# Performance work log

Measured on AMD Instinct MI355X. Metric: run time of the kernel, lower is better.

## Reference

```python
import jax, jax.numpy as jnp
import numpy as np


def setup_inputs() -> dict:
    key = jax.random.key(0)
    ks = jax.random.split(key, 5)
    B, T, I, H = 64, 512, 1024, 1024
    s = 1.0 / np.sqrt(H)
    return {
        "x": jax.random.normal(ks[0], (B, T, I), dtype=jnp.float32),
        "w_ih": jax.random.normal(ks[1], (4 * H, I), dtype=jnp.float32) * s,
        "b_ih": jax.random.normal(ks[2], (4 * H,), dtype=jnp.float32) * s,
        "w_hh": jax.random.normal(ks[3], (4 * H, H), dtype=jnp.float32) * s,
        "b_hh": jax.random.normal(ks[4], (4 * H,), dtype=jnp.float32) * s,
    }


def _lstm(x, w_ih, b_ih, w_hh, b_hh):
    B, T, _ = x.shape
    H = w_hh.shape[1]
    # Precompute input projections for all timesteps: [T, B, 4H]
    gx = jnp.einsum("bti,gi->tbg", x, w_ih) + b_ih
    h0 = jnp.zeros((B, H), dtype=x.dtype)
    c0 = jnp.zeros((B, H), dtype=x.dtype)

    def step(carry, g_x):
        h, c = carry
        gates = g_x + h @ w_hh.T + b_hh  # [B, 4H]
        i_lin, f_lin, g_lin, o_lin = jnp.split(gates, 4, axis=-1)
        i = jax.nn.sigmoid(i_lin)
        f = jax.nn.sigmoid(f_lin)
        g = jnp.tanh(g_lin)
        o = jax.nn.sigmoid(o_lin)
        c = f * c + i * g
        h = o * jnp.tanh(c)
        return (h, c), h

    (hT, cT), hs = jax.lax.scan(step, (h0, c0), gx)
    output = jnp.transpose(hs, (1, 0, 2))  # [B, T, H]
    hn = hT[None, :, :]  # [1, B, H]
    cn = cT[None, :, :]
    return output, hn, cn


def reference(x, w_ih, b_ih, w_hh, b_hh):
    return _lstm(x, w_ih, b_ih, w_hh, b_hh)
```

## Files before the change

### kernel.cpp

```cpp
#include <hip/hip_runtime.h>
#include <hip/hip_bf16.h>

#define Bv 64
#define Tv 512
#define Iv 1024
#define Hv 1024
#define G4v 4096
#define BH (Bv * Hv)
#define NHB 64
#define NXB 128
#define NBLK (NHB + NXB)
#define DEPTH 8
#define FSTR 16

typedef __attribute__((ext_vector_type(8))) short bf16x8;
typedef __attribute__((ext_vector_type(4))) float f32x4;

#define LOADC(p)    __hip_atomic_load((p), __ATOMIC_RELAXED, __HIP_MEMORY_SCOPE_AGENT)
#define STOREC(p,v) __hip_atomic_store((p), (v), __ATOMIC_RELAXED, __HIP_MEMORY_SCOPE_AGENT)

__device__ __forceinline__ float sigmoid_f(float v) { return 1.f / (1.f + __expf(-v)); }
__device__ __forceinline__ float tanh_f(float v) { return 1.f - 2.f / (__expf(2.f * v) + 1.f); }

__device__ __forceinline__ void store_short_sc1(void* p, unsigned short v) {
  asm volatile("global_store_short %0, %1, off sc1" :: "v"(p), "v"((unsigned)v) : "memory");
}

__global__ void prep(const float* __restrict__ w_ih, const float* __restrict__ w_hh,
                     const float* __restrict__ b_ih, const float* __restrict__ b_hh,
                     __hip_bfloat16* __restrict__ wbih, __hip_bfloat16* __restrict__ wbhh,
                     float* __restrict__ bias, __hip_bfloat16* __restrict__ hbuf,
                     unsigned* __restrict__ hflag, unsigned* __restrict__ xflag) {
  unsigned i = blockIdx.x * 256u + threadIdx.x;
  wbih[i] = __float2bfloat16(w_ih[i]);
  wbhh[i] = __float2bfloat16(w_hh[i]);
  if (i < (unsigned)G4v) bias[i] = b_ih[i] + b_hh[i];
  if (i < 2u * BH) hbuf[i] = __float2bfloat16(0.f);
  if (i < (unsigned)(NHB * FSTR)) hflag[i] = 0u;
  if (i < (unsigned)(NXB * FSTR)) xflag[i] = 0u;
}

__global__ void __launch_bounds__(256, 1) lstm_main(
    const float* __restrict__ x,
    const __hip_bfloat16* __restrict__ wbih,
    const __hip_bfloat16* __restrict__ wbhh,
    const float* __restrict__ bias,
    __hip_bfloat16* __restrict__ hbuf,
    float* __restrict__ xg,
    float* __restrict__ out,
    unsigned* __restrict__ hflag,
    unsigned* __restrict__ xflag,
    int ring)
{
  extern __shared__ char lds[];

  const int bid  = blockIdx.x;
  const bool is_h = (bid < NHB);
  const int tid  = threadIdx.x;
  const int lane = tid & 63;
  const int wave = tid >> 6;
  const int lrow = lane & 15;
  const int lkg  = lane >> 4;
  const int lk   = lkg * 8;

  const int wg = is_h ? bid : ((bid - NHB) >> 1);
  const int rh = is_h ? 0 : ((bid - NHB) & 1);

  {
    const __hip_bfloat16* wsrc = is_h ? wbhh : wbih;
    for (int c = tid; c < 8192; c += 256) {
      int n   = c >> 7;
      int k16 = c & 127;
      int gc  = ((n >> 4) << 10) + (wg << 4) + (n & 15);
      uint4 v = *(const uint4*)(wsrc + ((size_t)gc << 10) + (k16 << 3));
      unsigned byt = (unsigned)((n << 11) + (k16 << 4)) ^ ((unsigned)(n & 7) << 4);
      *(uint4*)(&lds[byt]) = v;
    }
  }
  __syncthreads();

  if (!is_h) {
    const int j  = bid - NHB;
    const int wr = wave & 1;
    const int wc = wave >> 1;
    const int arow = rh * 32 + wr * 16 + lrow;
    const float* xa = x + (size_t)arow * (Tv * Iv) + lk;

    for (int t = 0; t < Tv; ++t) {
      if (t >= DEPTH) {
        if (wave == 0) {
          const unsigned tgt = (unsigned)(t - DEPTH + 1);
          for (;;) {
            unsigned hf = LOADC(&hflag[lane * FSTR]);
            if (__all(hf >= tgt)) break;
            __builtin_amdgcn_s_sleep(4);
          }
        }
        __syncthreads();
        asm volatile("" ::: "memory");
      }
      f32x4 acc[2];
      acc[0] = f32x4{0.f,0.f,0.f,0.f}; acc[1] = f32x4{0.f,0.f,0.f,0.f};
      const float* xt = xa + (size_t)t * Iv;
      #pragma unroll 4
      for (int ks = 0; ks < 32; ++ks) {
        int k0 = (ks << 5) + lk;
        float4 f0 = *(const float4*)(xt + (ks << 5));
        float4 f1 = *(const float4*)(xt + (ks << 5) + 4);
        union { __hip_bfloat16 e[8]; bf16x8 v; } u;
        u.e[0] = __float2bfloat16(f0.x); u.e[1] = __float2bfloat16(f0.y);
        u.e[2] = __float2bfloat16(f0.z); u.e[3] = __float2bfloat16(f0.w);
        u.e[4] = __float2bfloat16(f1.x); u.e[5] = __float2bfloat16(f1.y);
        u.e[6] = __float2bfloat16(f1.z); u.e[7] = __float2bfloat16(f1.w);
        bf16x8 b0, b1;
        {
          int n = wc * 32 + lrow;
          unsigned byt = (unsigned)((n << 11) + (k0 << 1)) ^ ((unsigned)(n & 7) << 4);
          b0 = *(const bf16x8*)(&lds[byt]);
          n += 16;
          byt = (unsigned)((n << 11) + (k0 << 1)) ^ ((unsigned)(n & 7) << 4);
          b1 = *(const bf16x8*)(&lds[byt]);
        }
        acc[0] = __builtin_amdgcn_mfma_f32_16x16x32_bf16(u.v, b0, acc[0], 0, 0, 0);
        acc[1] = __builtin_amdgcn_mfma_f32_16x16x32_bf16(u.v, b1, acc[1], 0, 0, 0);
      }
      float* dst = xg + (size_t)(t & (DEPTH - 1)) * (Bv * G4v);
      for (int nf = 0; nf < 2; ++nf) {
        int gc  = (wc * 2 + nf) * 1024 + (wg << 4) + lrow;
        int row = rh * 32 + wr * 16 + (lkg << 2);
        for (int r = 0; r < 4; ++r)
          STOREC(&dst[(size_t)(row + r) * G4v + gc], acc[nf][r]);
      }
      asm volatile("s_waitcnt vmcnt(0)" ::: "memory");
      __syncthreads();
      if (tid == 0) STOREC(&xflag[j * FSTR], (unsigned)(t + 1));
      __syncthreads();
    }
    return;
  }

  const int orow0 = wave * 16 + (lkg << 2);
  const int ocol  = (wg << 4) + lrow;
  float c_state[4] = {0.f, 0.f, 0.f, 0.f};
  float biasv[4];
  #pragma unroll
  for (int g = 0; g < 4; ++g) biasv[g] = bias[(g << 10) + ocol];

  const int ar = wave * 16 + lrow;

  for (int t = 0; t < Tv; ++t) {
    if (wave == 0) {
      const unsigned ht = (unsigned)t, xtg = (unsigned)(t + 1);
      const unsigned* xf = &xflag[(2 * wg + (lane & 1)) * FSTR];
      for (;;) {
        unsigned hf = LOADC(&hflag[lane * FSTR]);
        unsigned xv = LOADC(xf);
        if (__all(hf >= ht && xv >= xtg)) break;
        __builtin_amdgcn_s_sleep(1);
      }
    }
    __syncthreads();
    asm volatile("" ::: "memory");
    f32x4 acc[4];
    for (int nf = 0; nf < 4; ++nf) acc[nf] = f32x4{0.f,0.f,0.f,0.f};
    bf16x8 aqv[32];
    const unsigned long long* hq = nullptr;
    if (ring) {
      const char* hrow = (const char*)(hbuf + (size_t)t * BH) + ((size_t)ar << 11) + (lkg << 4);
      #pragma unroll
      for (int ks = 0; ks < 32; ++ks)
        aqv[ks] = *(const bf16x8*)(hrow + (ks << 6));
    } else {
      hq = (const unsigned long long*)(hbuf + (size_t)(t & 1) * BH) + (size_t)ar * 256 + lkg * 2;
      #pragma unroll
      for (int ks = 0; ks < 32; ++ks) {
        union { unsigned long long q[2]; bf16x8 v; } ua;
        ua.q[0] = LOADC(hq + ks * 8);
        ua.q[1] = LOADC(hq + ks * 8 + 1);
        aqv[ks] = ua.v;
      }
    }
    float xgv[16];
    {
      const float* xgs = xg + (size_t)(t & (DEPTH - 1)) * (Bv * G4v);
      #pragma unroll
      for (int g = 0; g < 4; ++g)
        #pragma unroll
        for (int r = 0; r < 4; ++r)
          xgv[g * 4 + r] = LOADC(xgs + (size_t)(orow0 + r) * G4v + (g << 10) + ocol);
    }
    #pragma unroll
    for (int ks = 0; ks < 32; ++ks) {
      int k0 = (ks << 5) + lk;
      #pragma unroll
      for (int nf = 0; nf < 4; ++nf) {
        int n = nf * 16 + lrow;
        unsigned byt = (unsigned)((n << 11) + (k0 << 1)) ^ ((unsigned)(n & 7) << 4);
        bf16x8 b = *(const bf16x8*)(&lds[byt]);
        acc[nf] = __builtin_amdgcn_mfma_f32_16x16x32_bf16(aqv[ks], b, acc[nf], 0, 0, 0);
      }
    }
    float hv[4];
    #pragma unroll
    for (int r = 0; r < 4; ++r) {
      float g0 = acc[0][r] + xgv[0 + r]  + biasv[0];
      float g1 = acc[1][r] + xgv[4 + r]  + biasv[1];
      float g2 = acc[2][r] + xgv[8 + r]  + biasv[2];
      float g3 = acc[3][r] + xgv[12 + r] + biasv[3];
      float ig = sigmoid_f(g0);
      float fg = sigmoid_f(g1);
      float gg = tanh_f(g2);
      float og = sigmoid_f(g3);
      float cv = fg * c_state[r] + ig * gg;
      c_state[r] = cv;
      hv[r] = og * tanh_f(cv);
    }
    {
      __hip_bfloat16* hs = hbuf
          + (ring ? (size_t)(t + 1) * BH : (size_t)((t + 1) & 1) * BH) + ocol;
      #pragma unroll
      for (int r = 0; r < 4; ++r) {
        __hip_bfloat16 hb = __float2bfloat16(hv[r]);
        store_short_sc1(hs + ((size_t)(orow0 + r) << 10), *(unsigned short*)&hb);
      }
    }
    asm volatile("s_waitcnt vmcnt(0)" ::: "memory");
    __syncthreads();
    if (tid == 0) STOREC(&hflag[wg * FSTR], (unsigned)(t + 1));
    #pragma unroll
    for (int r = 0; r < 4; ++r) {
      float* ow = out + (size_t)(orow0 + r) * (Tv * Hv) + ((size_t)t << 10) + ocol;
      __builtin_nontemporal_store(hv[r], ow);
    }
    if (t == Tv - 1) {
      #pragma unroll
      for (int r = 0; r < 4; ++r) {
        float* hn = out + (size_t)Bv * Tv * Hv + ((size_t)(orow0 + r) << 10) + ocol;
        __builtin_nontemporal_store(hv[r], hn);
        __builtin_nontemporal_store(c_state[r], hn + BH);
      }
    }
  }
}

extern "C" void kernel_launch(void* const* d_in, const int* in_sizes, int n_in,
                              void* d_out, int out_size, void* d_ws, size_t ws_size,
                              hipStream_t stream) {
  const float* x    = (const float*)d_in[0];
  const float* w_ih = (const float*)d_in[1];
  const float* b_ih = (const float*)d_in[2];
  const float* w_hh = (const float*)d_in[3];
  const float* b_hh = (const float*)d_in[4];
  float* out = (float*)d_out;

  char* ws = (char*)d_ws;
  __hip_bfloat16* wbih = (__hip_bfloat16*)(ws);
  __hip_bfloat16* wbhh = (__hip_bfloat16*)(ws + ((size_t)8 << 20));
  float*          bias = (float*)(ws + ((size_t)16 << 20));
  float*          xg   = (float*)(ws + ((size_t)18 << 20));
  unsigned*       hflag= (unsigned*)(ws + ((size_t)26 << 20));
  unsigned*       xflag= (unsigned*)(ws + ((size_t)26 << 20) + 8192);

  const size_t ringBytes = (size_t)(Tv + 1) * BH * 2;
  const size_t needRing  = ((size_t)32 << 20) + ringBytes;
  const int ring = (ws_size >= needRing) ? 1 : 0;
  __hip_bfloat16* hbuf = ring
      ? (__hip_bfloat16*)(ws + ((size_t)32 << 20))
      : (__hip_bfloat16*)(ws + ((size_t)16 << 20) + 65536);

  hipLaunchKernelGGL(prep, dim3(16384), dim3(256), 0, stream,
                     w_ih, w_hh, b_ih, b_hh, wbih, wbhh, bias, hbuf, hflag, xflag);

  const unsigned ldsBytes = 131072u;
  hipFuncSetAttribute((const void*)lstm_main,
                      hipFuncAttributeMaxDynamicSharedMemorySize, (int)ldsBytes);

  const float* xA = x;
  const __hip_bfloat16* wbihA = wbih;
  const __hip_bfloat16* wbhhA = wbhh;
  const float* biasA = bias;
  __hip_bfloat16* hbufA = hbuf;
  float* xgA = xg;
  float* outA = out;
  unsigned* hflagA = hflag;
  unsigned* xflagA = xflag;
  int ringA = ring;
  void* args[10] = {(void*)&xA, (void*)&wbihA, (void*)&wbhhA, (void*)&biasA,
                    (void*)&hbufA, (void*)&xgA, (void*)&outA, (void*)&hflagA,
                    (void*)&xflagA, (void*)&ringA};

  hipError_t lerr = hipLaunchCooperativeKernel((const void*)lstm_main, dim3(NBLK),
                                               dim3(256), args, ldsBytes, stream);
  if (lerr != hipSuccess) {
    (void)hipGetLastError();
    hipLaunchKernelGGL(lstm_main, dim3(NBLK), dim3(256), ldsBytes, stream,
                       xA, wbihA, wbhhA, biasA, hbufA, xgA, outA, hflagA, xflagA, ringA);
  }
}
```

Measured before the change: 4.732 ms.

## Replace block-wide barriers with per-wave flags for batch-slice synchronization

Each wave of the recurrent blocks now owns a 16-row batch slice. It waits only on the h flags of the same slice across all 64 blocks and on its own x-projection flag, then publishes its own flag. This removes the __syncthreads barriers and the wave-0 polling per timestep, so waves in a block can progress independently. In exchange there are four times as many flags, more polling traffic, and the x-producer blocks must check all four slices.

```diff
diff --git a/kernel.cpp b/kernel.cpp
--- a/kernel.cpp
+++ b/kernel.cpp
@@ -36,7 +36,7 @@
   wbhh[i] = __float2bfloat16(w_hh[i]);
   if (i < (unsigned)G4v) bias[i] = b_ih[i] + b_hh[i];
   if (i < 2u * BH) hbuf[i] = __float2bfloat16(0.f);
-  if (i < (unsigned)(NHB * FSTR)) hflag[i] = 0u;
+  if (i < (unsigned)(4 * NHB * FSTR)) hflag[i] = 0u;
   if (i < (unsigned)(NXB * FSTR)) xflag[i] = 0u;
 }
 
@@ -91,8 +91,11 @@
         if (wave == 0) {
           const unsigned tgt = (unsigned)(t - DEPTH + 1);
           for (;;) {
-            unsigned hf = LOADC(&hflag[lane * FSTR]);
-            if (__all(hf >= tgt)) break;
+            unsigned a0 = LOADC(&hflag[(0 * 64 + lane) * FSTR]);
+            unsigned a1 = LOADC(&hflag[(1 * 64 + lane) * FSTR]);
+            unsigned a2 = LOADC(&hflag[(2 * 64 + lane) * FSTR]);
+            unsigned a3 = LOADC(&hflag[(3 * 64 + lane) * FSTR]);
+            if (__all(a0 >= tgt && a1 >= tgt && a2 >= tgt && a3 >= tgt)) break;
             __builtin_amdgcn_s_sleep(4);
           }
         }
@@ -139,39 +142,36 @@
     return;
   }
 
-  const int orow0 = wave * 16 + (lkg << 2);
+  const int s     = wave;
+  const int orow0 = s * 16 + (lkg << 2);
   const int ocol  = (wg << 4) + lrow;
+  const int ar    = s * 16 + lrow;
   float c_state[4] = {0.f, 0.f, 0.f, 0.f};
   float biasv[4];
   #pragma unroll
   for (int g = 0; g < 4; ++g) biasv[g] = bias[(g << 10) + ocol];
-
-  const int ar = wave * 16 + lrow;
+  const unsigned* myxf = &xflag[(2 * wg + (s >> 1)) * FSTR];
+  unsigned* myhf = &hflag[(s * 64 + wg) * FSTR];
 
   for (int t = 0; t < Tv; ++t) {
-    if (wave == 0) {
-      const unsigned ht = (unsigned)t, xtg = (unsigned)(t + 1);
-      const unsigned* xf = &xflag[(2 * wg + (lane & 1)) * FSTR];
-      for (;;) {
-        unsigned hf = LOADC(&hflag[lane * FSTR]);
-        unsigned xv = LOADC(xf);
-        if (__all(hf >= ht && xv >= xtg)) break;
-        __builtin_amdgcn_s_sleep(1);
-      }
-    }
-    __syncthreads();
+    for (;;) {
+      unsigned hf = LOADC(&hflag[(s * 64 + lane) * FSTR]);
+      unsigned xv = LOADC(myxf);
+      if (__all(hf >= (unsigned)t && xv >= (unsigned)(t + 1))) break;
+      __builtin_amdgcn_s_sleep(1);
+    }
     asm volatile("" ::: "memory");
     f32x4 acc[4];
     for (int nf = 0; nf < 4; ++nf) acc[nf] = f32x4{0.f,0.f,0.f,0.f};
     bf16x8 aqv[32];
-    const unsigned long long* hq = nullptr;
     if (ring) {
       const char* hrow = (const char*)(hbuf + (size_t)t * BH) + ((size_t)ar << 11) + (lkg << 4);
       #pragma unroll
       for (int ks = 0; ks < 32; ++ks)
         aqv[ks] = *(const bf16x8*)(hrow + (ks << 6));
     } else {
-      hq = (const unsigned long long*)(hbuf + (size_t)(t & 1) * BH) + (size_t)ar * 256 + lkg * 2;
+      const unsigned long long* hq =
+          (const unsigned long long*)(hbuf + (size_t)(t & 1) * BH) + (size_t)ar * 256 + lkg * 2;
       #pragma unroll
       for (int ks = 0; ks < 32; ++ks) {
         union { unsigned long long q[2]; bf16x8 v; } ua;
@@ -225,8 +225,7 @@
       }
     }
     asm volatile("s_waitcnt vmcnt(0)" ::: "memory");
-    __syncthreads();
-    if (tid == 0) STOREC(&hflag[wg * FSTR], (unsigned)(t + 1));
+    if (lane == 0) STOREC(myhf, (unsigned)(t + 1));
     #pragma unroll
     for (int r = 0; r < 4; ++r) {
       float* ow = out + (size_t)(orow0 + r) * (Tv * Hv) + ((size_t)t << 10) + ocol;
@@ -259,7 +258,7 @@
   float*          bias = (float*)(ws + ((size_t)16 << 20));
   float*          xg   = (float*)(ws + ((size_t)18 << 20));
   unsigned*       hflag= (unsigned*)(ws + ((size_t)26 << 20));
-  unsigned*       xflag= (unsigned*)(ws + ((size_t)26 << 20) + 8192);
+  unsigned*       xflag= (unsigned*)(ws + ((size_t)26 << 20) + 16384);
 
   const size_t ringBytes = (size_t)(Tv + 1) * BH * 2;
   const size_t needRing  = ((size_t)32 << 20) + ringBytes;
```

Result: slower. 4.962 ms (+4.9%).

## Fuse input projection into recurrent blocks, computed two steps ahead

Applied to the files above, without the earlier changes.

Removes the separate producer blocks that computed x·W_ih into a global ring buffer with flag handshakes. Each recurrent block now computes its own input-projection tile for step t+2 right after publishing h_t, keeping the results in registers. This eliminates the xg global round-trip and the xflag polling, but adds per-step GEMM work with global w_ih loads to the recurrent blocks and uses fewer CUs.

```diff
diff --git a/kernel.cpp b/kernel.cpp
--- a/kernel.cpp
+++ b/kernel.cpp
@@ -8,9 +8,6 @@
 #define G4v 4096
 #define BH (Bv * Hv)
 #define NHB 64
-#define NXB 128
-#define NBLK (NHB + NXB)
-#define DEPTH 8
 #define FSTR 16
 
 typedef __attribute__((ext_vector_type(8))) short bf16x8;
@@ -30,14 +27,13 @@
                      const float* __restrict__ b_ih, const float* __restrict__ b_hh,
                      __hip_bfloat16* __restrict__ wbih, __hip_bfloat16* __restrict__ wbhh,
                      float* __restrict__ bias, __hip_bfloat16* __restrict__ hbuf,
-                     unsigned* __restrict__ hflag, unsigned* __restrict__ xflag) {
+                     unsigned* __restrict__ hflag) {
   unsigned i = blockIdx.x * 256u + threadIdx.x;
   wbih[i] = __float2bfloat16(w_ih[i]);
   wbhh[i] = __float2bfloat16(w_hh[i]);
   if (i < (unsigned)G4v) bias[i] = b_ih[i] + b_hh[i];
   if (i < 2u * BH) hbuf[i] = __float2bfloat16(0.f);
   if (i < (unsigned)(NHB * FSTR)) hflag[i] = 0u;
-  if (i < (unsigned)(NXB * FSTR)) xflag[i] = 0u;
 }
 
 __global__ void __launch_bounds__(256, 1) lstm_main(
@@ -46,132 +42,85 @@
     const __hip_bfloat16* __restrict__ wbhh,
     const float* __restrict__ bias,
     __hip_bfloat16* __restrict__ hbuf,
-    float* __restrict__ xg,
     float* __restrict__ out,
     unsigned* __restrict__ hflag,
-    unsigned* __restrict__ xflag,
     int ring)
 {
   extern __shared__ char lds[];
 
-  const int bid  = blockIdx.x;
-  const bool is_h = (bid < NHB);
   const int tid  = threadIdx.x;
   const int lane = tid & 63;
   const int wave = tid >> 6;
   const int lrow = lane & 15;
   const int lkg  = lane >> 4;
   const int lk   = lkg * 8;
-
-  const int wg = is_h ? bid : ((bid - NHB) >> 1);
-  const int rh = is_h ? 0 : ((bid - NHB) & 1);
+  const int wg   = blockIdx.x;
 
   {
-    const __hip_bfloat16* wsrc = is_h ? wbhh : wbih;
     for (int c = tid; c < 8192; c += 256) {
       int n   = c >> 7;
       int k16 = c & 127;
       int gc  = ((n >> 4) << 10) + (wg << 4) + (n & 15);
-      uint4 v = *(const uint4*)(wsrc + ((size_t)gc << 10) + (k16 << 3));
+      uint4 v = *(const uint4*)(wbhh + ((size_t)gc << 10) + (k16 << 3));
       unsigned byt = (unsigned)((n << 11) + (k16 << 4)) ^ ((unsigned)(n & 7) << 4);
       *(uint4*)(&lds[byt]) = v;
     }
   }
   __syncthreads();
 
-  if (!is_h) {
-    const int j  = bid - NHB;
-    const int wr = wave & 1;
-    const int wc = wave >> 1;
-    const int arow = rh * 32 + wr * 16 + lrow;
-    const float* xa = x + (size_t)arow * (Tv * Iv) + lk;
-
-    for (int t = 0; t < Tv; ++t) {
-      if (t >= DEPTH) {
-        if (wave == 0) {
-          const unsigned tgt = (unsigned)(t - DEPTH + 1);
-          for (;;) {
-            unsigned hf = LOADC(&hflag[lane * FSTR]);
-            if (__all(hf >= tgt)) break;
-            __builtin_amdgcn_s_sleep(4);
-          }
-        }
-        __syncthreads();
-        asm volatile("" ::: "memory");
-      }
-      f32x4 acc[2];
-      acc[0] = f32x4{0.f,0.f,0.f,0.f}; acc[1] = f32x4{0.f,0.f,0.f,0.f};
-      const float* xt = xa + (size_t)t * Iv;
-      #pragma unroll 4
-      for (int ks = 0; ks < 32; ++ks) {
-        int k0 = (ks << 5) + lk;
-        float4 f0 = *(const float4*)(xt + (ks << 5));
-        float4 f1 = *(const float4*)(xt + (ks << 5) + 4);
-        union { __hip_bfloat16 e[8]; bf16x8 v; } u;
-        u.e[0] = __float2bfloat16(f0.x); u.e[1] = __float2bfloat16(f0.y);
-        u.e[2] = __float2bfloat16(f0.z); u.e[3] = __float2bfloat16(f0.w);
-        u.e[4] = __float2bfloat16(f1.x); u.e[5] = __float2bfloat16(f1.y);
-        u.e[6] = __float2bfloat16(f1.z); u.e[7] = __float2bfloat16(f1.w);
-        bf16x8 b0, b1;
-        {
-          int n = wc * 32 + lrow;
-          unsigned byt = (unsigned)((n << 11) + (k0 << 1)) ^ ((unsigned)(n & 7) << 4);
-          b0 = *(const bf16x8*)(&lds[byt]);
-          n += 16;
-          byt = (unsigned)((n << 11) + (k0 << 1)) ^ ((unsigned)(n & 7) << 4);
-          b1 = *(const bf16x8*)(&lds[byt]);
-        }
-        acc[0] = __builtin_amdgcn_mfma_f32_16x16x32_bf16(u.v, b0, acc[0], 0, 0, 0);
-        acc[1] = __builtin_amdgcn_mfma_f32_16x16x32_bf16(u.v, b1, acc[1], 0, 0, 0);
-      }
-      float* dst = xg + (size_t)(t & (DEPTH - 1)) * (Bv * G4v);
-      for (int nf = 0; nf < 2; ++nf) {
-        int gc  = (wc * 2 + nf) * 1024 + (wg << 4) + lrow;
-        int row = rh * 32 + wr * 16 + (lkg << 2);
-        for (int r = 0; r < 4; ++r)
-          STOREC(&dst[(size_t)(row + r) * G4v + gc], acc[nf][r]);
-      }
-      asm volatile("s_waitcnt vmcnt(0)" ::: "memory");
-      __syncthreads();
-      if (tid == 0) STOREC(&xflag[j * FSTR], (unsigned)(t + 1));
-      __syncthreads();
-    }
-    return;
-  }
-
   const int orow0 = wave * 16 + (lkg << 2);
   const int ocol  = (wg << 4) + lrow;
+  const int ar    = wave * 16 + lrow;
   float c_state[4] = {0.f, 0.f, 0.f, 0.f};
   float biasv[4];
   #pragma unroll
   for (int g = 0; g < 4; ++g) biasv[g] = bias[(g << 10) + ocol];
 
-  const int ar = wave * 16 + lrow;
-
-  for (int t = 0; t < Tv; ++t) {
+  auto xgemm = [&](int tx, f32x4 (&accx)[4]) {
+    #pragma unroll
+    for (int nf = 0; nf < 4; ++nf) accx[nf] = f32x4{0.f, 0.f, 0.f, 0.f};
+    const float* xt = x + (size_t)ar * (Tv * Iv) + (size_t)tx * Iv + lk;
+    #pragma unroll 4
+    for (int ks = 0; ks < 32; ++ks) {
+      float4 f0 = *(const float4*)(xt + (ks << 5));
+      float4 f1 = *(const float4*)(xt + (ks << 5) + 4);
+      union { __hip_bfloat16 e[8]; bf16x8 v; } u;
+      u.e[0] = __float2bfloat16(f0.x); u.e[1] = __float2bfloat16(f0.y);
+      u.e[2] = __float2bfloat16(f0.z); u.e[3] = __float2bfloat16(f0.w);
+      u.e[4] = __float2bfloat16(f1.x); u.e[5] = __float2bfloat16(f1.y);
+      u.e[6] = __float2bfloat16(f1.z); u.e[7] = __float2bfloat16(f1.w);
+      #pragma unroll
+      for (int nf = 0; nf < 4; ++nf) {
+        int gc = (nf << 10) + (wg << 4) + lrow;
+        bf16x8 b = *(const bf16x8*)(wbih + (size_t)gc * 1024 + (ks << 5) + lk);
+        accx[nf] = __builtin_amdgcn_mfma_f32_16x16x32_bf16(u.v, b, accx[nf], 0, 0, 0);
+      }
+    }
+  };
+
+  auto step_body = [&](int t, f32x4 (&accx)[4]) {
     if (wave == 0) {
-      const unsigned ht = (unsigned)t, xtg = (unsigned)(t + 1);
-      const unsigned* xf = &xflag[(2 * wg + (lane & 1)) * FSTR];
+      const unsigned ht = (unsigned)t;
       for (;;) {
         unsigned hf = LOADC(&hflag[lane * FSTR]);
-        unsigned xv = LOADC(xf);
-        if (__all(hf >= ht && xv >= xtg)) break;
+        if (__all(hf >= ht)) break;
         __builtin_amdgcn_s_sleep(1);
       }
     }
     __syncthreads();
     asm volatile("" ::: "memory");
     f32x4 acc[4];
-    for (int nf = 0; nf < 4; ++nf) acc[nf] = f32x4{0.f,0.f,0.f,0.f};
+    #pragma unroll
+    for (int nf = 0; nf < 4; ++nf) acc[nf] = f32x4{0.f, 0.f, 0.f, 0.f};
     bf16x8 aqv[32];
-    const unsigned long long* hq = nullptr;
     if (ring) {
       const char* hrow = (const char*)(hbuf + (size_t)t * BH) + ((size_t)ar << 11) + (lkg << 4);
       #pragma unroll
       for (int ks = 0; ks < 32; ++ks)
         aqv[ks] = *(const bf16x8*)(hrow + (ks << 6));
     } else {
-      hq = (const unsigned long long*)(hbuf + (size_t)(t & 1) * BH) + (size_t)ar * 256 + lkg * 2;
+      const unsigned long long* hq =
+          (const unsigned long long*)(hbuf + (size_t)(t & 1) * BH) + (size_t)ar * 256 + lkg * 2;
       #pragma unroll
       for (int ks = 0; ks < 32; ++ks) {
         union { unsigned long long q[2]; bf16x8 v; } ua;
@@ -180,15 +129,6 @@
         aqv[ks] = ua.v;
       }
     }
-    float xgv[16];
-    {
-      const float* xgs = xg + (size_t)(t & (DEPTH - 1)) * (Bv * G4v);
-      #pragma unroll
-      for (int g = 0; g < 4; ++g)
-        #pragma unroll
-        for (int r = 0; r < 4; ++r)
-          xgv[g * 4 + r] = LOADC(xgs + (size_t)(orow0 + r) * G4v + (g << 10) + ocol);
-    }
     #pragma unroll
     for (int ks = 0; ks < 32; ++ks) {
       int k0 = (ks << 5) + lk;
@@ -203,10 +143,10 @@
     float hv[4];
     #pragma unroll
     for (int r = 0; r < 4; ++r) {
-      float g0 = acc[0][r] + xgv[0 + r]  + biasv[0];
-      float g1 = acc[1][r] + xgv[4 + r]  + biasv[1];
-      float g2 = acc[2][r] + xgv[8 + r]  + biasv[2];
-      float g3 = acc[3][r] + xgv[12 + r] + biasv[3];
+      float g0 = (acc[0][r] + accx[0][r]) + biasv[0];
+      float g1 = (acc[1][r] + accx[1][r]) + biasv[1];
+      float g2 = (acc[2][r] + accx[2][r]) + biasv[2];
+      float g3 = (acc[3][r] + accx[3][r]) + biasv[3];
       float ig = sigmoid_f(g0);
       float fg = sigmoid_f(g1);
       float gg = tanh_f(g2);
@@ -240,6 +180,16 @@
         __builtin_nontemporal_store(c_state[r], hn + BH);
       }
     }
+    if (t + 2 < Tv) xgemm(t + 2, accx);
+  };
+
+  f32x4 accxA[4], accxB[4];
+  xgemm(0, accxA);
+  xgemm(1, accxB);
+
+  for (int t = 0; t < Tv; t += 2) {
+    step_body(t,     accxA);
+    step_body(t + 1, accxB);
   }
 }
 
@@ -257,9 +207,7 @@
   __hip_bfloat16* wbih = (__hip_bfloat16*)(ws);
   __hip_bfloat16* wbhh = (__hip_bfloat16*)(ws + ((size_t)8 << 20));
   float*          bias = (float*)(ws + ((size_t)16 << 20));
-  float*          xg   = (float*)(ws + ((size_t)18 << 20));
   unsigned*       hflag= (unsigned*)(ws + ((size_t)26 << 20));
-  unsigned*       xflag= (unsigned*)(ws + ((size_t)26 << 20) + 8192);
 
   const size_t ringBytes = (size_t)(Tv + 1) * BH * 2;
   const size_t needRing  = ((size_t)32 << 20) + ringBytes;
@@ -269,7 +217,7 @@
       : (__hip_bfloat16*)(ws + ((size_t)16 << 20) + 65536);
 
   hipLaunchKernelGGL(prep, dim3(16384), dim3(256), 0, stream,
-                     w_ih, w_hh, b_ih, b_hh, wbih, wbhh, bias, hbuf, hflag, xflag);
+                     w_ih, w_hh, b_ih, b_hh, wbih, wbhh, bias, hbuf, hflag);
 
   const unsigned ldsBytes = 131072u;
   hipFuncSetAttribute((const void*)lstm_main,
@@ -280,20 +228,17 @@
   const __hip_bfloat16* wbhhA = wbhh;
   const float* biasA = bias;
   __hip_bfloat16* hbufA = hbuf;
-  float* xgA = xg;
   float* outA = out;
   unsigned* hflagA = hflag;
-  unsigned* xflagA = xflag;
   int ringA = ring;
-  void* args[10] = {(void*)&xA, (void*)&wbihA, (void*)&wbhhA, (void*)&biasA,
-                    (void*)&hbufA, (void*)&xgA, (void*)&outA, (void*)&hflagA,
-                    (void*)&xflagA, (void*)&ringA};
-
-  hipError_t lerr = hipLaunchCooperativeKernel((const void*)lstm_main, dim3(NBLK),
+  void* args[8] = {(void*)&xA, (void*)&wbihA, (void*)&wbhhA, (void*)&biasA,
+                   (void*)&hbufA, (void*)&outA, (void*)&hflagA, (void*)&ringA};
+
+  hipError_t lerr = hipLaunchCooperativeKernel((const void*)lstm_main, dim3(NHB),
                                                dim3(256), args, ldsBytes, stream);
   if (lerr != hipSuccess) {
     (void)hipGetLastError();
-    hipLaunchKernelGGL(lstm_main, dim3(NBLK), dim3(256), ldsBytes, stream,
-                       xA, wbihA, wbhhA, biasA, hbufA, xgA, outA, hflagA, xflagA, ringA);
+    hipLaunchKernelGGL(lstm_main, dim3(NHB), dim3(256), ldsBytes, stream,
+                       xA, wbihA, wbhhA, biasA, hbufA, outA, hflagA, ringA);
   }
 }
```

After: 17.97 ms. 3.8x slower.
